# Kernel tuning notes

Measured on AMD Instinct MI355X. Metric: run time of the kernel, lower is better.

Reference implementation:

```python
import jax, jax.numpy as jnp
import numpy as np

B, S, E, H = 64, 512, 256, 512


def setup_inputs() -> dict:
    key = jax.random.key(0)
    ks = jax.random.split(key, 8)
    std_h = 1.0 / np.sqrt(H)
    std_e = 1.0 / np.sqrt(E)
    return {
        "inputs": jax.random.normal(ks[0], (B, S, E), dtype=jnp.float32),
        "timestamps": jax.random.uniform(ks[1], (B, S), dtype=jnp.float32) * 10.0,
        "W_all_w": jax.random.uniform(ks[2], (4 * H, H), jnp.float32, -std_h, std_h),
        "W_all_b": jax.random.uniform(ks[3], (4 * H,), jnp.float32, -std_h, std_h),
        "U_all_w": jax.random.uniform(ks[4], (4 * H, E), jnp.float32, -std_e, std_e),
        "U_all_b": jax.random.uniform(ks[5], (4 * H,), jnp.float32, -std_e, std_e),
        "W_d_w": jax.random.uniform(ks[6], (H, H), jnp.float32, -std_h, std_h),
        "W_d_b": jax.random.uniform(ks[7], (H,), jnp.float32, -std_h, std_h),
    }


def reference(inputs, timestamps, W_all_w, W_all_b, U_all_w, U_all_b, W_d_w, W_d_b):
    b, seq, embed = inputs.shape
    hidden = W_d_w.shape[0]
    # Precompute input projections for all steps: [b, seq, 4H]
    u_proj = jnp.einsum('bse,ge->bsg', inputs, U_all_w) + U_all_b
    # Time-decay factor per step: 1 / log(e + dt), shape [b, seq, 1]
    decay = (1.0 / jnp.log(jnp.float32(np.e) + timestamps))[..., None]

    def step(carry, xs):
        h, c = carry
        u_s, dec_s = xs  # [b, 4H], [b, 1]
        c_s1 = jnp.tanh(c @ W_d_w.T + W_d_b)
        c_adj = (c - c_s1) + c_s1 * dec_s
        outs = h @ W_all_w.T + W_all_b + u_s
        f, i, o, c_tmp = jnp.split(outs, 4, axis=1)
        f = jax.nn.sigmoid(f)
        i = jax.nn.sigmoid(i)
        o = jax.nn.sigmoid(o)
        c_tmp = jnp.tanh(c_tmp)
        c_new = f * c_adj + i * c_tmp
        h_new = o * jnp.tanh(c_new)
        return (h_new, c_new), h_new

    h0 = jnp.zeros((b, hidden), dtype=inputs.dtype)
    c0 = jnp.zeros((b, hidden), dtype=inputs.dtype)
    # scan over seq: move time to leading axis
    (h_f, c_f), hs = jax.lax.scan(
        step, (h0, c0),
        (jnp.swapaxes(u_proj, 0, 1), jnp.swapaxes(decay, 0, 1)))
    outputs = jnp.swapaxes(hs, 0, 1)  # [b, seq, H]
    return outputs, h_f, c_f
```

## Files before the change

kernel.cpp:

```cpp
#include <hip/hip_runtime.h>
#include <cmath>


typedef short bf16x8 __attribute__((ext_vector_type(8)));
typedef float f32x4  __attribute__((ext_vector_type(4)));

#define Bdim 64
#define Sdim 512
#define Edim 256
#define Hdim 512
#define NWG  64
#define NT   512
#define FSTR 16

#define WS_FLAGS 0
#define WS_HMIR0 16384
#define WS_HMIR1 (WS_HMIR0 + 65536)
#define WS_CMIR0 (WS_HMIR1 + 65536)
#define WS_CMIR1 (WS_CMIR0 + 65536)
#define WS_WFRAG (WS_CMIR1 + 65536)
#define WS_DFRAG (WS_WFRAG + 3145728)

__device__ __forceinline__ unsigned ld_dev_u32(const unsigned* p) {
    return __hip_atomic_load(p, __ATOMIC_RELAXED, __HIP_MEMORY_SCOPE_AGENT);
}
__device__ __forceinline__ void st_dev_u32(unsigned* p, unsigned v) {
    __hip_atomic_store(p, v, __ATOMIC_RELAXED, __HIP_MEMORY_SCOPE_AGENT);
}
__device__ __forceinline__ unsigned long long ld_dev_u64(const unsigned long long* p) {
    return __hip_atomic_load(p, __ATOMIC_RELAXED, __HIP_MEMORY_SCOPE_AGENT);
}
__device__ __forceinline__ unsigned short f2bf(float f) {
    union { float f; unsigned u; } v; v.f = f;
    return (unsigned short)((v.u + 0x7FFFu + ((v.u >> 16) & 1u)) >> 16);
}
__device__ __forceinline__ unsigned pack2(float lo, float hi) {
    return (unsigned)f2bf(lo) | ((unsigned)f2bf(hi) << 16);
}
__device__ __forceinline__ float fast_tanh(float x) {
    const float ax = __builtin_fabsf(x);
    const float e  = __expf(-2.0f * ax);
    const float t  = (1.0f - e) / (1.0f + e);
    return __builtin_copysignf(t, x);
}
__device__ __forceinline__ float fast_sigmoid(float x) {
    return 1.0f / (1.0f + __expf(-x));
}

__global__ __launch_bounds__(256) void tlstm_prep(
    const float* __restrict__ Wall, const float* __restrict__ Uall,
    const float* __restrict__ Wd, unsigned char* __restrict__ ws)
{
    const int w = blockIdx.x, t = threadIdx.x;
    unsigned short* Wfrag = (unsigned short*)(ws + WS_WFRAG);
    unsigned short* Dfrag = (unsigned short*)(ws + WS_DFRAG);
    const int l = t & 63, ks = t >> 6, nn = l & 15, q = l >> 4;

    if (w < 128) {
        const int cg = w >> 3, wv = w & 7;
        const int G = wv * 16 + nn, g = G >> 5, jj = G & 31;
        const int row = g * Hdim + cg * 32 + jj;
        for (int i = 0; i < 6; ++i) {
            const int kp = ks * 6 + i;
            const float* src = (kp < 16)
                ? Wall + (size_t)row * Hdim + kp * 32 + q * 8
                : Uall + (size_t)row * Edim + (kp - 16) * 32 + q * 8;
            unsigned* dst = (unsigned*)(Wfrag
                + (((size_t)(cg * 8 + wv) * 24 + kp) * 64 + l) * 8);
            #pragma unroll
            for (int p = 0; p < 4; ++p) dst[p] = pack2(src[2*p], src[2*p+1]);
        }
    } else if (w < 192) {
        const int u = w - 128, cg = u >> 2, q4 = u & 3;
        for (int half = 0; half < 2; ++half) {
            const int wv = q4 * 2 + half;
            const int i  = ks;
            const int dt = wv >> 2, kd = (wv & 3) * 4 + i;
            const int row = cg * 32 + dt * 16 + nn;
            const float* src = Wd + (size_t)row * Hdim + kd * 32 + q * 8;
            unsigned* dst = (unsigned*)(Dfrag
                + (((size_t)(cg * 8 + wv) * 4 + i) * 64 + l) * 8);
            #pragma unroll
            for (int p = 0; p < 4; ++p) dst[p] = pack2(src[2*p], src[2*p+1]);
        }
    } else {
        const int idx = (w - 192) * 256 + t;
        uint4* z = (uint4*)ws;
        for (int i = idx; i < 17408; i += 16384) z[i] = make_uint4(0, 0, 0, 0);
    }
}

__global__ __launch_bounds__(NT, 2) void tlstm_mfma(
    const float* __restrict__ x,
    const float* __restrict__ ts,
    const float* __restrict__ Wall_b,
    const float* __restrict__ Uall_b,
    const float* __restrict__ Wd_b,
    float* __restrict__ out,
    unsigned char* __restrict__ ws)
{
    __shared__ __align__(16) unsigned short h_sb[16 * 520];
    __shared__ __align__(16) unsigned short c_sb[16 * 520];
    __shared__ __align__(16) unsigned short x_sb[16 * 264];
    __shared__ float Dred[2][4][256];
    __shared__ float act[4 * 512];
    __shared__ float cs1v[512];
    __shared__ float decv[16];

    int* flags = (int*)(ws + WS_FLAGS);
    const unsigned short* Wfrag = (const unsigned short*)(ws + WS_WFRAG);
    const unsigned short* Dfrag = (const unsigned short*)(ws + WS_DFRAG);

    const int t    = threadIdx.x;
    const int bg   = blockIdx.x >> 4, cg = blockIdx.x & 15;
    const int b0   = bg * 16, j0 = cg * 32;
    const int w    = t >> 6, lane = t & 63, q = lane >> 4, nn = lane & 15;

    const int G = w * 16 + nn, g = G >> 5, jj = G & 31;
    const float bias_g = Wall_b[g * Hdim + j0 + jj] + Uall_b[g * Hdim + j0 + jj];
    const int rtl = t >> 8, rpos = t & 255, rm = rpos >> 4, rn = rpos & 15;
    const float bias_d = Wd_b[j0 + rtl * 16 + rn];
    const int fm = t >> 5, fj = t & 31;

    bf16x8 bw[24];
    #pragma unroll
    for (int i = 0; i < 24; ++i)
        bw[i] = *(const bf16x8*)(Wfrag
            + (((size_t)(cg * 8 + w) * 24 + i) * 64 + lane) * 8);
    bf16x8 bd[4];
    #pragma unroll
    for (int i = 0; i < 4; ++i)
        bd[i] = *(const bf16x8*)(Dfrag
            + (((size_t)(cg * 8 + w) * 4 + i) * 64 + lane) * 8);

    const int srow = t >> 5, sc32 = t & 31;

    auto stage_x = [&](int sx) {
        const float4* xp = (const float4*)(x + ((size_t)(b0 + srow) * Sdim + sx) * Edim + sc32 * 8);
        float4 v0 = xp[0], v1 = xp[1];
        *(uint4*)((unsigned*)x_sb + srow * 132 + sc32 * 4) =
            make_uint4(pack2(v0.x, v0.y), pack2(v0.z, v0.w),
                       pack2(v1.x, v1.y), pack2(v1.z, v1.w));
    };

    float c_reg = 0.0f;
    stage_x(0);

    for (int s = 0;; ++s) {
        {
            const unsigned long long* hsrc =
                (const unsigned long long*)(ws + WS_HMIR0 + (s & 1) * 65536);
            const unsigned long long* csrc =
                (const unsigned long long*)(ws + WS_CMIR0 + (s & 1) * 65536);
            const int goff = ((b0 + srow) * 256 + sc32 * 8) >> 1;
            unsigned long long hv[4], cv[4];
            #pragma unroll
            for (int i = 0; i < 4; ++i) hv[i] = ld_dev_u64(hsrc + goff + i);
            #pragma unroll
            for (int i = 0; i < 4; ++i) cv[i] = ld_dev_u64(csrc + goff + i);
            unsigned* hls = (unsigned*)h_sb + srow * 260 + sc32 * 8;
            unsigned* cls = (unsigned*)c_sb + srow * 260 + sc32 * 8;
            ((ulonglong2*)hls)[0] = make_ulonglong2(hv[0], hv[1]);
            ((ulonglong2*)hls)[1] = make_ulonglong2(hv[2], hv[3]);
            ((ulonglong2*)cls)[0] = make_ulonglong2(cv[0], cv[1]);
            ((ulonglong2*)cls)[1] = make_ulonglong2(cv[2], cv[3]);
        }
        __syncthreads();

        f32x4 acc0 = {0.f, 0.f, 0.f, 0.f}, acc1 = {0.f, 0.f, 0.f, 0.f};
        f32x4 accd = {0.f, 0.f, 0.f, 0.f};
        #pragma unroll
        for (int i = 0; i < 12; ++i) {
            bf16x8 av = *(const bf16x8*)(h_sb + nn * 520 + i * 32 + q * 8);
            acc0 = __builtin_amdgcn_mfma_f32_16x16x32_bf16(av, bw[i], acc0, 0, 0, 0);
        }
        #pragma unroll
        for (int i = 12; i < 24; ++i) {
            const unsigned short* asrc = (i < 16)
                ? (h_sb + nn * 520 + i * 32 + q * 8)
                : (x_sb + nn * 264 + (i - 16) * 32 + q * 8);
            bf16x8 av = *(const bf16x8*)asrc;
            acc1 = __builtin_amdgcn_mfma_f32_16x16x32_bf16(av, bw[i], acc1, 0, 0, 0);
        }
        #pragma unroll
        for (int i = 0; i < 4; ++i) {
            const int kd = (w & 3) * 4 + i;
            bf16x8 av = *(const bf16x8*)(c_sb + nn * 520 + kd * 32 + q * 8);
            accd = __builtin_amdgcn_mfma_f32_16x16x32_bf16(av, bd[i], accd, 0, 0, 0);
        }

        const int dt = w >> 2;
        #pragma unroll
        for (int r = 0; r < 4; ++r) {
            const int m = q * 4 + r;
            const float sv = acc0[r] + acc1[r] + bias_g;
            act[g * 512 + m * 32 + jj] = (g == 3) ? fast_tanh(sv) : fast_sigmoid(sv);
            Dred[dt][w & 3][m * 16 + ((nn + m) & 15)] = accd[r];
        }
        __syncthreads();

        {
            const int sl = rm * 16 + ((rn + rm) & 15);
            const float sv = Dred[rtl][0][sl] + Dred[rtl][1][sl]
                           + Dred[rtl][2][sl] + Dred[rtl][3][sl];
            cs1v[rm * 32 + rtl * 16 + rn] = fast_tanh(sv + bias_d);
        }
        if (t < 16)
            decv[t] = 1.0f / __logf(2.7182818284590452f + ts[(b0 + t) * Sdim + s]);
        __syncthreads();

        {
            const float dec  = decv[fm];
            const float cs1  = cs1v[t];
            const float cadj = (c_reg - cs1) + cs1 * dec;
            const float f  = act[t];
            const float ii = act[512 + t];
            const float oo = act[1024 + t];
            const float gg = act[1536 + t];
            const float cn = f * cadj + ii * gg;
            const float hn = oo * fast_tanh(cn);
            c_reg = cn;
            out[((size_t)(b0 + fm) * Sdim + s) * Hdim + j0 + fj] = hn;
            const float hn1 = __shfl_down(hn, 1);
            const float cn1 = __shfl_down(cn, 1);
            if (s < Sdim - 1) {
                if ((t & 1) == 0) {
                    unsigned* hmw = (unsigned*)(ws + WS_HMIR0 + ((s + 1) & 1) * 65536);
                    unsigned* cmw = (unsigned*)(ws + WS_CMIR0 + ((s + 1) & 1) * 65536);
                    const int didx = ((b0 + fm) * Hdim + j0 + fj) >> 1;
                    st_dev_u32(hmw + didx, pack2(hn, hn1));
                    st_dev_u32(cmw + didx, pack2(cn, cn1));
                }
            } else {
                float* hf = out + (size_t)Bdim * Sdim * Hdim;
                float* cf = hf + (size_t)Bdim * Hdim;
                hf[(b0 + fm) * Hdim + j0 + fj] = hn;
                cf[(b0 + fm) * Hdim + j0 + fj] = cn;
            }
        }

        if (s == Sdim - 1) break;

        __syncthreads();
        if (t == 0)
            __hip_atomic_store(&flags[blockIdx.x * FSTR], s + 1,
                               __ATOMIC_RELAXED, __HIP_MEMORY_SCOPE_AGENT);
        stage_x(s + 1);
        if (t < 16) {
            while (__hip_atomic_load(&flags[(bg * 16 + t) * FSTR],
                                     __ATOMIC_RELAXED,
                                     __HIP_MEMORY_SCOPE_AGENT) < s + 1) {
                __builtin_amdgcn_s_sleep(1);
            }
        }
        __syncthreads();
    }
}

extern "C" void kernel_launch(void* const* d_in, const int* in_sizes, int n_in,
                              void* d_out, int out_size, void* d_ws, size_t ws_size,
                              hipStream_t stream) {
    const float* x      = (const float*)d_in[0];
    const float* ts     = (const float*)d_in[1];
    const float* Wall   = (const float*)d_in[2];
    const float* Wall_b = (const float*)d_in[3];
    const float* Uall   = (const float*)d_in[4];
    const float* Uall_b = (const float*)d_in[5];
    const float* Wd     = (const float*)d_in[6];
    const float* Wd_b   = (const float*)d_in[7];

    tlstm_prep<<<256, 256, 0, stream>>>(Wall, Uall, Wd, (unsigned char*)d_ws);
    tlstm_mfma<<<NWG, NT, 0, stream>>>(x, ts, Wall_b, Uall_b, Wd_b,
                                       (float*)d_out, (unsigned char*)d_ws);
}
```

Measured before the change: 2.008 ms.

## Overlap x-projection MFMAs with state loads and fuse decay/tanh into cell update

Issues the global h/c mirror loads before the x-part MFMAs so that the input-projection matrix products overlap the load latency. It also removes one __syncthreads per step by computing the W_d reduction, tanh and decay directly in the cell-update threads instead of staging them through shared memory. The per-step output store is moved after the flag publish so it does not delay the signal to peer blocks. Each thread now does a redundant log per step, and the extra sync after stage_x(0) is needed because x_sb is read before the first barrier.

```diff
diff --git a/kernel.cpp b/kernel.cpp
--- a/kernel.cpp
+++ b/kernel.cpp
@@ -104,8 +104,6 @@
     __shared__ __align__(16) unsigned short x_sb[16 * 264];
     __shared__ float Dred[2][4][256];
     __shared__ float act[4 * 512];
-    __shared__ float cs1v[512];
-    __shared__ float decv[16];
 
     int* flags = (int*)(ws + WS_FLAGS);
     const unsigned short* Wfrag = (const unsigned short*)(ws + WS_WFRAG);
@@ -118,9 +116,9 @@
 
     const int G = w * 16 + nn, g = G >> 5, jj = G & 31;
     const float bias_g = Wall_b[g * Hdim + j0 + jj] + Uall_b[g * Hdim + j0 + jj];
-    const int rtl = t >> 8, rpos = t & 255, rm = rpos >> 4, rn = rpos & 15;
-    const float bias_d = Wd_b[j0 + rtl * 16 + rn];
     const int fm = t >> 5, fj = t & 31;
+    const int fdt = fj >> 4, fn = fj & 15;
+    const float bias_d = Wd_b[j0 + fj];
 
     bf16x8 bw[24];
     #pragma unroll
@@ -143,21 +141,30 @@
                        pack2(v1.x, v1.y), pack2(v1.z, v1.w));
     };
 
+    stage_x(0);
     float c_reg = 0.0f;
-    stage_x(0);
+    __syncthreads();
 
     for (int s = 0;; ++s) {
+        const unsigned long long* hsrc =
+            (const unsigned long long*)(ws + WS_HMIR0 + (s & 1) * 65536);
+        const unsigned long long* csrc =
+            (const unsigned long long*)(ws + WS_CMIR0 + (s & 1) * 65536);
+        const size_t goff = (size_t)(b0 + srow) * 128 + sc32 * 4;
+        unsigned long long hv[4], cv[4];
+        #pragma unroll
+        for (int i = 0; i < 4; ++i) hv[i] = ld_dev_u64(hsrc + goff + i);
+        #pragma unroll
+        for (int i = 0; i < 4; ++i) cv[i] = ld_dev_u64(csrc + goff + i);
+
+        f32x4 acc1 = {0.f, 0.f, 0.f, 0.f};
+        #pragma unroll
+        for (int i = 16; i < 24; ++i) {
+            bf16x8 av = *(const bf16x8*)(x_sb + nn * 264 + (i - 16) * 32 + q * 8);
+            acc1 = __builtin_amdgcn_mfma_f32_16x16x32_bf16(av, bw[i], acc1, 0, 0, 0);
+        }
+
         {
-            const unsigned long long* hsrc =
-                (const unsigned long long*)(ws + WS_HMIR0 + (s & 1) * 65536);
-            const unsigned long long* csrc =
-                (const unsigned long long*)(ws + WS_CMIR0 + (s & 1) * 65536);
-            const int goff = ((b0 + srow) * 256 + sc32 * 8) >> 1;
-            unsigned long long hv[4], cv[4];
-            #pragma unroll
-            for (int i = 0; i < 4; ++i) hv[i] = ld_dev_u64(hsrc + goff + i);
-            #pragma unroll
-            for (int i = 0; i < 4; ++i) cv[i] = ld_dev_u64(csrc + goff + i);
             unsigned* hls = (unsigned*)h_sb + srow * 260 + sc32 * 8;
             unsigned* cls = (unsigned*)c_sb + srow * 260 + sc32 * 8;
             ((ulonglong2*)hls)[0] = make_ulonglong2(hv[0], hv[1]);
@@ -167,7 +174,7 @@
         }
         __syncthreads();
 
-        f32x4 acc0 = {0.f, 0.f, 0.f, 0.f}, acc1 = {0.f, 0.f, 0.f, 0.f};
+        f32x4 acc0 = {0.f, 0.f, 0.f, 0.f};
         f32x4 accd = {0.f, 0.f, 0.f, 0.f};
         #pragma unroll
         for (int i = 0; i < 12; ++i) {
@@ -175,11 +182,8 @@
             acc0 = __builtin_amdgcn_mfma_f32_16x16x32_bf16(av, bw[i], acc0, 0, 0, 0);
         }
         #pragma unroll
-        for (int i = 12; i < 24; ++i) {
-            const unsigned short* asrc = (i < 16)
-                ? (h_sb + nn * 520 + i * 32 + q * 8)
-                : (x_sb + nn * 264 + (i - 16) * 32 + q * 8);
-            bf16x8 av = *(const bf16x8*)asrc;
+        for (int i = 12; i < 16; ++i) {
+            bf16x8 av = *(const bf16x8*)(h_sb + nn * 520 + i * 32 + q * 8);
             acc1 = __builtin_amdgcn_mfma_f32_16x16x32_bf16(av, bw[i], acc1, 0, 0, 0);
         }
         #pragma unroll
@@ -191,36 +195,33 @@
 
         const int dt = w >> 2;
         #pragma unroll
-        for (int r = 0; r < 4; ++r) {
-            const int m = q * 4 + r;
-            const float sv = acc0[r] + acc1[r] + bias_g;
-            act[g * 512 + m * 32 + jj] = (g == 3) ? fast_tanh(sv) : fast_sigmoid(sv);
-            Dred[dt][w & 3][m * 16 + ((nn + m) & 15)] = accd[r];
-        }
-        __syncthreads();
-
+        for (int rr = 0; rr < 4; ++rr) {
+            const int m = q * 4 + rr;
+            const float sv = acc0[rr] + acc1[rr] + bias_g;
+            act[g * 512 + m * 32 + jj] =
+                (g == 3) ? fast_tanh(sv) : fast_sigmoid(sv);
+            Dred[dt][w & 3][m * 16 + ((nn + m) & 15)] = accd[rr];
+        }
+        __syncthreads();
+
+        float hn;
+        size_t out_idx;
         {
-            const int sl = rm * 16 + ((rn + rm) & 15);
-            const float sv = Dred[rtl][0][sl] + Dred[rtl][1][sl]
-                           + Dred[rtl][2][sl] + Dred[rtl][3][sl];
-            cs1v[rm * 32 + rtl * 16 + rn] = fast_tanh(sv + bias_d);
-        }
-        if (t < 16)
-            decv[t] = 1.0f / __logf(2.7182818284590452f + ts[(b0 + t) * Sdim + s]);
-        __syncthreads();
-
-        {
-            const float dec  = decv[fm];
-            const float cs1  = cs1v[t];
+            const int sl = fm * 16 + ((fn + fm) & 15);
+            const float dsum = Dred[fdt][0][sl] + Dred[fdt][1][sl]
+                             + Dred[fdt][2][sl] + Dred[fdt][3][sl];
+            const float cs1  = fast_tanh(dsum + bias_d);
+            const float dec  = 1.0f / __logf(2.7182818284590452f
+                                             + ts[(size_t)(b0 + fm) * Sdim + s]);
             const float cadj = (c_reg - cs1) + cs1 * dec;
             const float f  = act[t];
             const float ii = act[512 + t];
             const float oo = act[1024 + t];
             const float gg = act[1536 + t];
             const float cn = f * cadj + ii * gg;
-            const float hn = oo * fast_tanh(cn);
+            hn = oo * fast_tanh(cn);
             c_reg = cn;
-            out[((size_t)(b0 + fm) * Sdim + s) * Hdim + j0 + fj] = hn;
+            out_idx = ((size_t)(b0 + fm) * Sdim + s) * Hdim + j0 + fj;
             const float hn1 = __shfl_down(hn, 1);
             const float cn1 = __shfl_down(cn, 1);
             if (s < Sdim - 1) {
@@ -232,6 +233,7 @@
                     st_dev_u32(cmw + didx, pack2(cn, cn1));
                 }
             } else {
+                out[out_idx] = hn;
                 float* hf = out + (size_t)Bdim * Sdim * Hdim;
                 float* cf = hf + (size_t)Bdim * Hdim;
                 hf[(b0 + fm) * Hdim + j0 + fj] = hn;
@@ -243,8 +245,9 @@
 
         __syncthreads();
         if (t == 0)
-            __hip_atomic_store(&flags[blockIdx.x * FSTR], s + 1,
-                               __ATOMIC_RELAXED, __HIP_MEMORY_SCOPE_AGENT);
+            st_dev_u32((unsigned*)&flags[(bg * 16 + cg) * FSTR],
+                       (unsigned)(s + 1));
+        out[out_idx] = hn;
         stage_x(s + 1);
         if (t < 16) {
             while (__hip_atomic_load(&flags[(bg * 16 + t) * FSTR],
```

Result: faster. 1.837 ms (-8.5%).
